# Kernel optimization log

Hardware: AMD Instinct MI355X
Metric: run time of the kernel (lower is better)

The kernel has to match this reference:

```python
import jax, jax.numpy as jnp
import numpy as np


def _hardswish(x):
    # torch.nn.Hardswish: x * relu6(x + 3) / 6
    return x * jnp.clip(x + 3.0, 0.0, 6.0) * (1.0 / 6.0)


def _local_linear(x, W, b):
    # x: [B, N, G*ig], W: [G, og, ig], b: [G, og]
    # Faithful to torch Local_Linear: split -> per-group Linear -> unsqueeze(-1)
    # -> cat on last dim -> flatten(2). The cat/flatten interleaves groups:
    # out[..., o*G + g] = y[..., g, o].
    B, N, C = x.shape
    G, og, ig = W.shape
    xg = x.reshape(B, N, G, ig)
    y = jnp.einsum('bngi,goi->bngo', xg, W) + b  # [B, N, G, og]
    return jnp.transpose(y, (0, 1, 3, 2)).reshape(B, N, og * G)


def setup_inputs() -> dict:
    key = jax.random.key(0)
    ks = jax.random.split(key, 5)
    B, N, C = 8, 2048, 1152
    G = 9
    hid = 4608
    ig1, og1 = C // G, hid // G      # 128, 512
    ig2, og2 = hid // G, C // G      # 512, 128
    x = jax.random.normal(ks[0], (B, N, C), dtype=jnp.float32)
    W1 = jax.random.normal(ks[1], (G, og1, ig1), dtype=jnp.float32) * (1.0 / np.sqrt(ig1))
    b1 = jax.random.normal(ks[2], (G, og1), dtype=jnp.float32) * 0.01
    W2 = jax.random.normal(ks[3], (G, og2, ig2), dtype=jnp.float32) * (1.0 / np.sqrt(ig2))
    b2 = jax.random.normal(ks[4], (G, og2), dtype=jnp.float32) * 0.01
    return {"x": x, "W1": W1, "b1": b1, "W2": W2, "b2": b2}


def reference(x, W1, b1, W2, b2):
    h = _local_linear(x, W1, b1)   # [B, N, 4608] (interleaved group layout)
    h = _hardswish(h)
    out = _local_linear(h, W2, b2)  # [B, N, 1152]
    return out
```

## Files before the change

### kernel.cpp

```cpp
#include <hip/hip_runtime.h>

typedef short bf16x8 __attribute__((ext_vector_type(8)));
typedef float f32x4 __attribute__((ext_vector_type(4)));

#define NG   9
#define CIN  1152
#define IG1  128
#define OG1  512
#define IG2  512
#define OG2  128
#define KP   576
#define HROW 5184
#define MTOT 16384
#define OSTRIDE 1156

__device__ __forceinline__ short f2bf(float f) {
    unsigned u = __float_as_uint(f);
    u += 0x7fff + ((u >> 16) & 1);
    return (short)(u >> 16);
}

__global__ __launch_bounds__(256) void prep_w1(const float* __restrict__ w1, short* __restrict__ w1b) {
    int i = blockIdx.x * 256 + threadIdx.x;
    if (i < NG * OG1 * IG1) w1b[i] = f2bf(w1[i]);
}

__global__ __launch_bounds__(256) void prep_w2(const float* __restrict__ w2, short* __restrict__ w2p) {
    int i = blockIdx.x * 256 + threadIdx.x;
    if (i >= NG * OG2 * KP) return;
    int g2  = i / (OG2 * KP);
    int rem = i - g2 * (OG2 * KP);
    int o2  = rem / KP;
    int kp  = rem - o2 * KP;
    int g1 = kp >> 6, r = kp & 63;
    int olo = (512 * g2 - g1 + 8) / 9;
    int j = 9 * (olo + r) + g1 - 512 * g2;
    float v = (j < 512) ? w2[(g2 * OG2 + o2) * IG2 + j] : 0.0f;
    w2p[i] = f2bf(v);
}

__global__ __launch_bounds__(256) void k1(const float* __restrict__ x, const short* __restrict__ w1b,
                                          const float* __restrict__ b1, short* __restrict__ hbuf) {
    __shared__ short As[128 * 16 * 8];
    __shared__ short Bs[64 * 16 * 8];
    const int t = threadIdx.x;
    const int mt = blockIdx.x, g1 = blockIdx.y;
    const int m0 = mt * 128;

    for (int i = 0; i < 8; ++i) {
        int flat = (i * 256 + t) * 8;
        int row = flat >> 7, col = flat & 127;
        const float* gp = x + (size_t)(m0 + row) * CIN + g1 * IG1 + col;
        float4 v0 = *(const float4*)gp;
        float4 v1 = *(const float4*)(gp + 4);
        bf16x8 s;
        s[0]=f2bf(v0.x); s[1]=f2bf(v0.y); s[2]=f2bf(v0.z); s[3]=f2bf(v0.w);
        s[4]=f2bf(v1.x); s[5]=f2bf(v1.y); s[6]=f2bf(v1.z); s[7]=f2bf(v1.w);
        int g = col >> 3;
        *(bf16x8*)&As[(row * 16 + (g ^ (row & 7))) * 8] = s;
    }

    const int lane = t & 63, w = t >> 6;
    const int wr = w >> 1, wc = w & 1;
    const int lr = lane & 15, lg = lane >> 4;

    for (int nt = 0; nt < 8; ++nt) {
        __syncthreads();
        for (int i = 0; i < 4; ++i) {
            int flat = (i * 256 + t) * 8;
            int row = flat >> 7, col = flat & 127;
            bf16x8 s = *(const bf16x8*)(w1b + ((g1 * OG1 + nt * 64 + row) * IG1 + col));
            int g = col >> 3;
            *(bf16x8*)&Bs[(row * 16 + (g ^ (row & 7))) * 8] = s;
        }
        __syncthreads();

        f32x4 acc[4][2];
        for (int mi = 0; mi < 4; ++mi) for (int ni = 0; ni < 2; ++ni) acc[mi][ni] = (f32x4){0.f,0.f,0.f,0.f};
        for (int kk = 0; kk < 4; ++kk) {
            int gk = kk * 4 + lg;
            bf16x8 af[4], bfr[2];
            for (int mi = 0; mi < 4; ++mi) {
                int row = wr * 64 + mi * 16 + lr;
                af[mi] = *(const bf16x8*)&As[(row * 16 + (gk ^ (row & 7))) * 8];
            }
            for (int ni = 0; ni < 2; ++ni) {
                int rb = wc * 32 + ni * 16 + lr;
                bfr[ni] = *(const bf16x8*)&Bs[(rb * 16 + (gk ^ (rb & 7))) * 8];
            }
            for (int mi = 0; mi < 4; ++mi)
                for (int ni = 0; ni < 2; ++ni)
                    acc[mi][ni] = __builtin_amdgcn_mfma_f32_16x16x32_bf16(af[mi], bfr[ni], acc[mi][ni], 0, 0, 0);
        }

        for (int ni = 0; ni < 2; ++ni) {
            int o = nt * 64 + wc * 32 + ni * 16 + lr;
            float bias = b1[g1 * OG1 + o];
            int c  = 9 * o + g1;
            int g2 = c >> 9;
            int olo = (512 * g2 - g1 + 8) / 9;
            int hcol = g2 * KP + (g1 << 6) + (o - olo);
            for (int mi = 0; mi < 4; ++mi) {
                for (int q = 0; q < 4; ++q) {
                    int row = m0 + wr * 64 + mi * 16 + lg * 4 + q;
                    float v = acc[mi][ni][q] + bias;
                    v = v * fminf(fmaxf(v + 3.0f, 0.0f), 6.0f) * (1.0f / 6.0f);
                    hbuf[(size_t)row * HROW + hcol] = f2bf(v);
                }
            }
        }
    }
}

__global__ __launch_bounds__(576) void k2(const short* __restrict__ hbuf, const short* __restrict__ w2p,
                                          const float* __restrict__ b2, float* __restrict__ out) {
    __shared__ float outs[32 * OSTRIDE];
    const int t = threadIdx.x;
    const int m0 = blockIdx.x * 32;
    const int g2 = t >> 6;
    const int lane = t & 63;
    const int lr = lane & 15, lg = lane >> 4;

    f32x4 acc[2][8];
#pragma unroll
    for (int mi = 0; mi < 2; ++mi)
#pragma unroll
        for (int nc = 0; nc < 8; ++nc) acc[mi][nc] = (f32x4){0.f, 0.f, 0.f, 0.f};

    const short* Ab = hbuf + (size_t)(m0 + lr) * HROW + g2 * KP + lg * 8;
    const short* Bb = w2p + (size_t)(g2 * OG2 + lr) * KP + lg * 8;

    for (int ks = 0; ks < 3; ++ks) {
        bf16x8 af[2][6];
#pragma unroll
        for (int mi = 0; mi < 2; ++mi)
#pragma unroll
            for (int kf = 0; kf < 6; ++kf)
                af[mi][kf] = *(const bf16x8*)(Ab + mi * 16 * HROW + (ks * 6 + kf) * 32);
#pragma unroll
        for (int kf = 0; kf < 6; ++kf) {
            bf16x8 bv[8];
#pragma unroll
            for (int nc = 0; nc < 8; ++nc)
                bv[nc] = *(const bf16x8*)(Bb + nc * 16 * KP + (ks * 6 + kf) * 32);
#pragma unroll
            for (int nc = 0; nc < 8; ++nc)
#pragma unroll
                for (int mi = 0; mi < 2; ++mi)
                    acc[mi][nc] = __builtin_amdgcn_mfma_f32_16x16x32_bf16(af[mi][kf], bv[nc], acc[mi][nc], 0, 0, 0);
        }
    }

#pragma unroll
    for (int nc = 0; nc < 8; ++nc) {
        int o2 = nc * 16 + lr;
        float bias = b2[g2 * OG2 + o2];
        int c = o2 * 9 + g2;
#pragma unroll
        for (int mi = 0; mi < 2; ++mi)
#pragma unroll
            for (int q = 0; q < 4; ++q)
                outs[(mi * 16 + lg * 4 + q) * OSTRIDE + c] = acc[mi][nc][q] + bias;
    }
    __syncthreads();

#pragma unroll
    for (int i = 0; i < 16; ++i) {
        int f4 = i * 576 + t;
        int row = f4 / 288;
        int c4 = f4 - row * 288;
        float4 v = *(const float4*)&outs[row * OSTRIDE + c4 * 4];
        *(float4*)&out[(size_t)(m0 + row) * CIN + c4 * 4] = v;
    }
}

extern "C" void kernel_launch(void* const* d_in, const int* in_sizes, int n_in,
                              void* d_out, int out_size, void* d_ws, size_t ws_size,
                              hipStream_t stream) {
    const float* x  = (const float*)d_in[0];
    const float* w1 = (const float*)d_in[1];
    const float* b1 = (const float*)d_in[2];
    const float* w2 = (const float*)d_in[3];
    const float* b2 = (const float*)d_in[4];
    float* out = (float*)d_out;

    short* hbuf = (short*)d_ws;
    short* w1b  = (short*)((char*)d_ws + (size_t)MTOT * HROW * 2);
    short* w2p  = (short*)((char*)d_ws + (size_t)MTOT * HROW * 2 + (size_t)NG * OG1 * IG1 * 2);

    prep_w1<<<(NG * OG1 * IG1 + 255) / 256, 256, 0, stream>>>(w1, w1b);
    prep_w2<<<(NG * OG2 * KP + 255) / 256, 256, 0, stream>>>(w2, w2p);
    k1<<<dim3(MTOT / 128, NG), 256, 0, stream>>>(x, w1b, b1, hbuf);
    k2<<<MTOT / 32, 576, 0, stream>>>(hbuf, w2p, b2, out);
}
```

Measured before the change: 200.1 us.

## Fuse both grouped linears into one kernel keeping hidden activations in LDS

Replaces the two-kernel pipeline (k1 writing a bf16 hidden buffer to global memory, k2 reading it back) with a single fused kernel. Each 512-thread block handles 32 rows: it stages x in LDS as bf16, then for each first-layer group computes a slice of hidden activations into a swizzled LDS tile and immediately accumulates that slice into the second-layer outputs. This removes the round trip of the large intermediate through HBM. In exchange, weights are read straight from global memory without LDS staging, there are more barriers per group, and the large LDS footprint limits occupancy.

```diff
diff --git a/kernel.cpp b/kernel.cpp
--- a/kernel.cpp
+++ b/kernel.cpp
@@ -10,9 +10,8 @@
 #define IG2  512
 #define OG2  128
 #define KP   576
-#define HROW 5184
+#define MT   32
 #define MTOT 16384
-#define OSTRIDE 1156
 
 __device__ __forceinline__ short f2bf(float f) {
     unsigned u = __float_as_uint(f);
@@ -39,138 +38,140 @@
     w2p[i] = f2bf(v);
 }
 
-__global__ __launch_bounds__(256) void k1(const float* __restrict__ x, const short* __restrict__ w1b,
-                                          const float* __restrict__ b1, short* __restrict__ hbuf) {
-    __shared__ short As[128 * 16 * 8];
-    __shared__ short Bs[64 * 16 * 8];
+__global__ __launch_bounds__(512) void fused(const float* __restrict__ x,
+                                             const short* __restrict__ w1b, const float* __restrict__ b1,
+                                             const short* __restrict__ w2p, const float* __restrict__ b2,
+                                             float* __restrict__ out) {
+    __shared__ __attribute__((aligned(16))) char smem[110592];
+    short* xs = (short*)smem;
+    short* ht = (short*)(smem + 73728);
+    float* outs = (float*)smem;
+
     const int t = threadIdx.x;
-    const int mt = blockIdx.x, g1 = blockIdx.y;
-    const int m0 = mt * 128;
+    const int m0 = blockIdx.x * MT;
+    const int w = t >> 6, lane = t & 63, lr = lane & 15, lg = lane >> 4;
 
-    for (int i = 0; i < 8; ++i) {
-        int flat = (i * 256 + t) * 8;
-        int row = flat >> 7, col = flat & 127;
-        const float* gp = x + (size_t)(m0 + row) * CIN + g1 * IG1 + col;
+    {
+        int2 z = {0, 0};
+#pragma unroll
+        for (int i = 0; i < 9; ++i) *(int2*)(ht + (i * 512 + t) * 4) = z;
+    }
+#pragma unroll
+    for (int i = 0; i < 9; ++i) {
+        int f = i * 512 + t;
+        int row = f / 144, c8 = f - row * 144;
+        const float* gp = x + (size_t)(m0 + row) * CIN + c8 * 8;
         float4 v0 = *(const float4*)gp;
         float4 v1 = *(const float4*)(gp + 4);
         bf16x8 s;
         s[0]=f2bf(v0.x); s[1]=f2bf(v0.y); s[2]=f2bf(v0.z); s[3]=f2bf(v0.w);
         s[4]=f2bf(v1.x); s[5]=f2bf(v1.y); s[6]=f2bf(v1.z); s[7]=f2bf(v1.w);
-        int g = col >> 3;
-        *(bf16x8*)&As[(row * 16 + (g ^ (row & 7))) * 8] = s;
+        *(bf16x8*)(xs + (row * 144 + (c8 ^ (row & 7))) * 8) = s;
     }
 
-    const int lane = t & 63, w = t >> 6;
-    const int wr = w >> 1, wc = w & 1;
-    const int lr = lane & 15, lg = lane >> 4;
+    f32x4 acc2[2][8];
+    f32x4 acc2b[2];
+#pragma unroll
+    for (int mi = 0; mi < 2; ++mi) {
+#pragma unroll
+        for (int ni = 0; ni < 8; ++ni) acc2[mi][ni] = (f32x4){0.f,0.f,0.f,0.f};
+        acc2b[mi] = (f32x4){0.f,0.f,0.f,0.f};
+    }
+    __syncthreads();
 
-    for (int nt = 0; nt < 8; ++nt) {
-        __syncthreads();
-        for (int i = 0; i < 4; ++i) {
-            int flat = (i * 256 + t) * 8;
-            int row = flat >> 7, col = flat & 127;
-            bf16x8 s = *(const bf16x8*)(w1b + ((g1 * OG1 + nt * 64 + row) * IG1 + col));
-            int g = col >> 3;
-            *(bf16x8*)&Bs[(row * 16 + (g ^ (row & 7))) * 8] = s;
+    for (int g1 = 0; g1 < NG; ++g1) {
+        f32x4 acc1[4][2];
+#pragma unroll
+        for (int oi = 0; oi < 4; ++oi)
+#pragma unroll
+            for (int mi = 0; mi < 2; ++mi) acc1[oi][mi] = (f32x4){0.f,0.f,0.f,0.f};
+#pragma unroll
+        for (int kf = 0; kf < 4; ++kf) {
+            bf16x8 bx[2];
+#pragma unroll
+            for (int mi = 0; mi < 2; ++mi) {
+                int row = mi * 16 + lr;
+                bx[mi] = *(const bf16x8*)(xs + (row * 144 + ((g1 * 16 + kf * 4 + lg) ^ (row & 7))) * 8);
+            }
+#pragma unroll
+            for (int oi = 0; oi < 4; ++oi) {
+                bf16x8 af = *(const bf16x8*)(w1b + ((size_t)(g1 * OG1 + w * 64 + oi * 16 + lr) * IG1 + kf * 32 + lg * 8));
+#pragma unroll
+                for (int mi = 0; mi < 2; ++mi)
+                    acc1[oi][mi] = __builtin_amdgcn_mfma_f32_16x16x32_bf16(af, bx[mi], acc1[oi][mi], 0, 0, 0);
+            }
         }
         __syncthreads();
-
-        f32x4 acc[4][2];
-        for (int mi = 0; mi < 4; ++mi) for (int ni = 0; ni < 2; ++ni) acc[mi][ni] = (f32x4){0.f,0.f,0.f,0.f};
-        for (int kk = 0; kk < 4; ++kk) {
-            int gk = kk * 4 + lg;
-            bf16x8 af[4], bfr[2];
-            for (int mi = 0; mi < 4; ++mi) {
-                int row = wr * 64 + mi * 16 + lr;
-                af[mi] = *(const bf16x8*)&As[(row * 16 + (gk ^ (row & 7))) * 8];
-            }
-            for (int ni = 0; ni < 2; ++ni) {
-                int rb = wc * 32 + ni * 16 + lr;
-                bfr[ni] = *(const bf16x8*)&Bs[(rb * 16 + (gk ^ (rb & 7))) * 8];
-            }
-            for (int mi = 0; mi < 4; ++mi)
-                for (int ni = 0; ni < 2; ++ni)
-                    acc[mi][ni] = __builtin_amdgcn_mfma_f32_16x16x32_bf16(af[mi], bfr[ni], acc[mi][ni], 0, 0, 0);
-        }
-
-        for (int ni = 0; ni < 2; ++ni) {
-            int o = nt * 64 + wc * 32 + ni * 16 + lr;
-            float bias = b1[g1 * OG1 + o];
-            int c  = 9 * o + g1;
-            int g2 = c >> 9;
-            int olo = (512 * g2 - g1 + 8) / 9;
-            int hcol = g2 * KP + (g1 << 6) + (o - olo);
-            for (int mi = 0; mi < 4; ++mi) {
-                for (int q = 0; q < 4; ++q) {
-                    int row = m0 + wr * 64 + mi * 16 + lg * 4 + q;
-                    float v = acc[mi][ni][q] + bias;
+#pragma unroll
+        for (int oi = 0; oi < 4; ++oi) {
+            int ob = w * 64 + oi * 16 + lg * 4;
+            float4 bias = *(const float4*)(b1 + g1 * OG1 + ob);
+#pragma unroll
+            for (int q = 0; q < 4; ++q) {
+                int o  = ob + q;
+                int c  = 9 * o + g1;
+                int g2 = c >> 9;
+                int olo = (512 * g2 - g1 + 8) / 9;
+                int hc = g2 * 64 + (o - olo);
+#pragma unroll
+                for (int mi = 0; mi < 2; ++mi) {
+                    int m = mi * 16 + lr;
+                    float v = acc1[oi][mi][q] + ((const float*)&bias)[q];
                     v = v * fminf(fmaxf(v + 3.0f, 0.0f), 6.0f) * (1.0f / 6.0f);
-                    hbuf[(size_t)row * HROW + hcol] = f2bf(v);
+                    *(short*)((char*)ht + m * 1152 + (((hc >> 3) ^ (m & 7)) << 4) + (hc & 7) * 2) = f2bf(v);
                 }
             }
         }
-    }
-}
-
-__global__ __launch_bounds__(576) void k2(const short* __restrict__ hbuf, const short* __restrict__ w2p,
-                                          const float* __restrict__ b2, float* __restrict__ out) {
-    __shared__ float outs[32 * OSTRIDE];
-    const int t = threadIdx.x;
-    const int m0 = blockIdx.x * 32;
-    const int g2 = t >> 6;
-    const int lane = t & 63;
-    const int lr = lane & 15, lg = lane >> 4;
-
-    f32x4 acc[2][8];
+        __syncthreads();
 #pragma unroll
-    for (int mi = 0; mi < 2; ++mi)
+        for (int kf = 0; kf < 2; ++kf) {
+            bf16x8 a_[2], a8_[2];
 #pragma unroll
-        for (int nc = 0; nc < 8; ++nc) acc[mi][nc] = (f32x4){0.f, 0.f, 0.f, 0.f};
-
-    const short* Ab = hbuf + (size_t)(m0 + lr) * HROW + g2 * KP + lg * 8;
-    const short* Bb = w2p + (size_t)(g2 * OG2 + lr) * KP + lg * 8;
-
-    for (int ks = 0; ks < 3; ++ks) {
-        bf16x8 af[2][6];
+            for (int mi = 0; mi < 2; ++mi) {
+                int m = mi * 16 + lr;
+                a_[mi]  = *(const bf16x8*)((char*)ht + m * 1152 + (((w * 8 + kf * 4 + lg) ^ (m & 7)) << 4));
+                a8_[mi] = *(const bf16x8*)((char*)ht + m * 1152 + (((64 + kf * 4 + lg) ^ (m & 7)) << 4));
+            }
 #pragma unroll
-        for (int mi = 0; mi < 2; ++mi)
-#pragma unroll
-            for (int kf = 0; kf < 6; ++kf)
-                af[mi][kf] = *(const bf16x8*)(Ab + mi * 16 * HROW + (ks * 6 + kf) * 32);
-#pragma unroll
-        for (int kf = 0; kf < 6; ++kf) {
-            bf16x8 bv[8];
-#pragma unroll
-            for (int nc = 0; nc < 8; ++nc)
-                bv[nc] = *(const bf16x8*)(Bb + nc * 16 * KP + (ks * 6 + kf) * 32);
-#pragma unroll
-            for (int nc = 0; nc < 8; ++nc)
+            for (int ni = 0; ni < 8; ++ni) {
+                bf16x8 bfr = *(const bf16x8*)(w2p + (size_t)(w * 128 + ni * 16 + lr) * KP + g1 * 64 + kf * 32 + lg * 8);
 #pragma unroll
                 for (int mi = 0; mi < 2; ++mi)
-                    acc[mi][nc] = __builtin_amdgcn_mfma_f32_16x16x32_bf16(af[mi][kf], bv[nc], acc[mi][nc], 0, 0, 0);
+                    acc2[mi][ni] = __builtin_amdgcn_mfma_f32_16x16x32_bf16(a_[mi], bfr, acc2[mi][ni], 0, 0, 0);
+            }
+            bf16x8 b8 = *(const bf16x8*)(w2p + (size_t)(8 * 128 + w * 16 + lr) * KP + g1 * 64 + kf * 32 + lg * 8);
+#pragma unroll
+            for (int mi = 0; mi < 2; ++mi)
+                acc2b[mi] = __builtin_amdgcn_mfma_f32_16x16x32_bf16(a8_[mi], b8, acc2b[mi], 0, 0, 0);
         }
     }
 
 #pragma unroll
-    for (int nc = 0; nc < 8; ++nc) {
-        int o2 = nc * 16 + lr;
-        float bias = b2[g2 * OG2 + o2];
-        int c = o2 * 9 + g2;
+    for (int h = 0; h < 2; ++h) {
+        __syncthreads();
 #pragma unroll
-        for (int mi = 0; mi < 2; ++mi)
+        for (int ni = 0; ni < 8; ++ni) {
+            float bias = b2[w * OG2 + ni * 16 + lr];
+            int c = (ni * 16 + lr) * 9 + w;
 #pragma unroll
             for (int q = 0; q < 4; ++q)
-                outs[(mi * 16 + lg * 4 + q) * OSTRIDE + c] = acc[mi][nc][q] + bias;
-    }
-    __syncthreads();
-
+                outs[(lg * 4 + q) * 1156 + c] = acc2[h][ni][q] + bias;
+        }
+        {
+            float bias8 = b2[8 * OG2 + w * 16 + lr];
+            int c8 = (w * 16 + lr) * 9 + 8;
 #pragma unroll
-    for (int i = 0; i < 16; ++i) {
-        int f4 = i * 576 + t;
-        int row = f4 / 288;
-        int c4 = f4 - row * 288;
-        float4 v = *(const float4*)&outs[row * OSTRIDE + c4 * 4];
-        *(float4*)&out[(size_t)(m0 + row) * CIN + c4 * 4] = v;
+            for (int q = 0; q < 4; ++q)
+                outs[(lg * 4 + q) * 1156 + c8] = acc2b[h][q] + bias8;
+        }
+        __syncthreads();
+#pragma unroll
+        for (int i = 0; i < 9; ++i) {
+            int f4 = i * 512 + t;
+            int row = f4 / 288, c4 = f4 - row * 288;
+            float4 v = *(const float4*)&outs[row * 1156 + c4 * 4];
+            *(float4*)&out[(size_t)(m0 + h * 16 + row) * CIN + c4 * 4] = v;
+        }
     }
 }
 
@@ -184,12 +185,10 @@
     const float* b2 = (const float*)d_in[4];
     float* out = (float*)d_out;
 
-    short* hbuf = (short*)d_ws;
-    short* w1b  = (short*)((char*)d_ws + (size_t)MTOT * HROW * 2);
-    short* w2p  = (short*)((char*)d_ws + (size_t)MTOT * HROW * 2 + (size_t)NG * OG1 * IG1 * 2);
+    short* w1b = (short*)d_ws;
+    short* w2p = (short*)((char*)d_ws + (size_t)NG * OG1 * IG1 * 2);
 
     prep_w1<<<(NG * OG1 * IG1 + 255) / 256, 256, 0, stream>>>(w1, w1b);
     prep_w2<<<(NG * OG2 * KP + 255) / 256, 256, 0, stream>>>(w2, w2p);
-    k1<<<dim3(MTOT / 128, NG), 256, 0, stream>>>(x, w1b, b1, hbuf);
-    k2<<<MTOT / 32, 576, 0, stream>>>(hbuf, w2p, b2, out);
+    fused<<<MTOT / MT, 512, 0, stream>>>(x, w1b, b1, w2p, b2, out);
 }
```

Result: slower. 228.3 us (+14.1%).
